# Kernel optimization log

Hardware: AMD Instinct MI355X
Metric: run time of the kernel (lower is better)

Reference implementation:

```python
import jax, jax.numpy as jnp
import numpy as np

B, N, F_IN, F_OUT = 8, 2048, 64, 64
ALPHA = 0.2
NEG = -9e15


def setup_inputs() -> dict:
    key = jax.random.key(0)
    k1, k2, k3, k4 = jax.random.split(key, 4)
    h = jax.random.normal(k1, (B, N, F_IN), dtype=jnp.float32)
    adj = jax.random.randint(k2, (N, N), 0, 2).astype(jnp.float32)
    W = jax.random.normal(k3, (F_OUT, F_IN), dtype=jnp.float32) * 0.05
    a = jax.random.normal(k4, (2 * F_OUT,), dtype=jnp.float32) * 0.05
    return {"h": h, "adj": adj, "W": W, "a": a}


def reference(h, adj, W, a):
    # Wh = h @ W^T  : [B, N, F_OUT]
    Wh = jnp.einsum("bnf,of->bno", h, W)
    # a([Wh_i, Wh_j]) decomposes exactly into a1.Wh_i + a2.Wh_j
    e1 = Wh @ a[:F_OUT]          # [B, N] contribution of source node i
    e2 = Wh @ a[F_OUT:]          # [B, N] contribution of target node j
    e = jax.nn.leaky_relu(e1[:, :, None] + e2[:, None, :], negative_slope=ALPHA)
    att = jnp.where(adj[None, :, :] > 0, e, NEG)
    att = jax.nn.softmax(att, axis=-1)   # [B, N, N]
    h_prime = jnp.einsum("bij,bjo->bio", att, Wh)
    return jax.nn.elu(h_prime)
```

## Files before the change

### kernel.cpp

```cpp
#include <hip/hip_runtime.h>
#include <hip/hip_bf16.h>
#include <math.h>


#define NN 2048
#define BB 8
#define ALPHA 0.2f

typedef __attribute__((ext_vector_type(8))) short s8v;
typedef __attribute__((ext_vector_type(4))) float f4v;

static __device__ __forceinline__ unsigned pk_bf16(float lo, float hi) {
  __hip_bfloat162 t = __float22bfloat162_rn(float2{lo, hi});
  return *(unsigned*)&t;
}

__global__ __launch_bounds__(256) void k_adj(const float* __restrict__ adj,
                                             unsigned long long* __restrict__ adjq) {
  const int t = threadIdx.x, lane = t & 63, w = t >> 6;
  const int row = blockIdx.x * 2 + (w >> 1);
  const int half = w & 1;
  const float* ar = adj + (size_t)row * NN + half * 1024;
  unsigned long long* aq = adjq + row * 32 + half * 16;
  #pragma unroll
  for (int it = 0; it < 16; ++it) {
    unsigned long long m = __ballot(ar[it * 64 + lane] > 0.f);
    if (lane == 0) aq[it] = m;
  }
}

__global__ __launch_bounds__(256, 2) void k_wh(
    const float* __restrict__ h, const float* __restrict__ W,
    const float* __restrict__ a, unsigned short* __restrict__ whtg,
    float* __restrict__ e1, float* __restrict__ e2) {
  __shared__ __align__(16) float hs[32][68];
  __shared__ __align__(16) unsigned short Ws[64][40];
  const int t = threadIdx.x, lane = t & 63, w = t >> 6;
  const int rowBase = blockIdx.x * 32;
  const int b = rowBase >> 11, n0 = rowBase & (NN - 1);

  float wr[64];
  #pragma unroll
  for (int k = 0; k < 16; ++k)
    *(f4v*)&wr[k * 4] = *(const f4v*)&W[lane * 64 + k * 4];

  #pragma unroll
  for (int qq = 0; qq < 2; ++qq) {
    const int idx = t + 256 * qq;
    const int r = idx >> 4, c = (idx & 15) * 4;
    *(f4v*)&hs[r][c] = *(const f4v*)&h[(size_t)(rowBase + r) * 64 + c];
  }
  const float a1v = a[lane], a2v = a[64 + lane];
  __syncthreads();

  const int r0 = w * 8;
  float acc[8];
  #pragma unroll
  for (int rr = 0; rr < 8; ++rr) acc[rr] = 0.f;
  #pragma unroll
  for (int f4i = 0; f4i < 16; ++f4i) {
    f4v hv[8];
    #pragma unroll
    for (int rr = 0; rr < 8; ++rr)
      hv[rr] = *(const f4v*)&hs[r0 + rr][f4i * 4];
    #pragma unroll
    for (int x = 0; x < 4; ++x) {
      const float wv = wr[f4i * 4 + x];
      #pragma unroll
      for (int rr = 0; rr < 8; ++rr) acc[rr] = fmaf(hv[rr][x], wv, acc[rr]);
    }
  }
  #pragma unroll
  for (int p = 0; p < 4; ++p)
    *(unsigned*)&Ws[lane][r0 + p * 2] = pk_bf16(acc[p * 2], acc[p * 2 + 1]);

  float s1[8], s2[8];
  #pragma unroll
  for (int rr = 0; rr < 8; ++rr) { s1[rr] = acc[rr] * a1v; s2[rr] = acc[rr] * a2v; }
  #pragma unroll
  for (int m = 1; m < 64; m <<= 1)
    #pragma unroll
    for (int rr = 0; rr < 8; ++rr) {
      s1[rr] += __shfl_xor(s1[rr], m);
      s2[rr] += __shfl_xor(s2[rr], m);
    }
  if (lane == 0)
    #pragma unroll
    for (int rr = 0; rr < 8; ++rr) {
      e1[rowBase + r0 + rr] = s1[rr];
      e2[rowBase + r0 + rr] = s2[rr];
    }
  __syncthreads();

  const int o = t >> 2, seg = t & 3;
  const s8v v = *(const s8v*)&Ws[o][seg * 8];
  *(s8v*)(whtg + ((size_t)(b * 64 + o) << 11) + n0 + seg * 8) = v;
}

__global__ __launch_bounds__(256, 2) void k_attn(
    const unsigned long long* __restrict__ adjq,
    const unsigned short* __restrict__ whtg,
    const float* __restrict__ e1g, const float* __restrict__ e2g,
    float* __restrict__ out) {
  __shared__ __align__(16) float e2row[NN];
  __shared__ __align__(16) float pc[4][16][68];
  __shared__ float ls[4][16];

  const int t = threadIdx.x, lane = t & 63, w = t >> 6;
  const int q = lane >> 4, l15 = lane & 15;
  const int b = blockIdx.y;
  const int i0 = blockIdx.x * 16;
  const size_t bN = (size_t)b * NN;

  #pragma unroll
  for (int kk = 0; kk < 2; ++kk) {
    const int idx = (t + 256 * kk) * 4;
    *(f4v*)&e2row[idx] = *(const f4v*)&e2g[bN + idx];
  }

  const float e1v = e1g[bN + i0 + l15];
  const unsigned long long* arow = adjq + (size_t)(i0 + l15) * 32 + w * 8;
  const unsigned short* wb = whtg + ((size_t)b << 17);
  const int jbase = w * 512;

  f4v acc[4];
  #pragma unroll
  for (int s = 0; s < 4; ++s) acc[s] = f4v{0.f, 0.f, 0.f, 0.f};
  float psum = 0.f;

  s8v bf[8];
  #pragma unroll
  for (int s = 0; s < 4; ++s)
    #pragma unroll
    for (int ks = 0; ks < 2; ++ks)
      bf[s * 2 + ks] =
          *(const s8v*)(wb + (((size_t)(s * 16 + l15)) << 11) + jbase + ks * 32 + q * 8);
  unsigned long long am = arow[0];

  __syncthreads();

  #pragma unroll
  for (int k = 0; k < 8; ++k) {
    const int j0 = jbase + k * 64;
    s8v cur[8];
    #pragma unroll
    for (int x = 0; x < 8; ++x) cur[x] = bf[x];
    const unsigned long long amc = am;
    if (k < 7) {
      const int jn = j0 + 64;
      #pragma unroll
      for (int s = 0; s < 4; ++s)
        #pragma unroll
        for (int ks = 0; ks < 2; ++ks)
          bf[s * 2 + ks] =
              *(const s8v*)(wb + (((size_t)(s * 16 + l15)) << 11) + jn + ks * 32 + q * 8);
      am = arow[k + 1];
    }

    s8v af[2];
    #pragma unroll
    for (int ks = 0; ks < 2; ++ks) {
      const unsigned bits = (unsigned)(amc >> (ks * 32 + q * 8)) & 0xffu;
      const f4v ea = *(const f4v*)&e2row[j0 + ks * 32 + q * 8];
      const f4v eb = *(const f4v*)&e2row[j0 + ks * 32 + q * 8 + 4];
      float p[8];
      #pragma unroll
      for (int jj = 0; jj < 8; ++jj) {
        const float s = e1v + (jj < 4 ? ea[jj & 3] : eb[jj & 3]);
        const float lr = fmaxf(s, ALPHA * s);
        const float pv = ((bits >> jj) & 1u) ? __expf(lr) : 0.f;
        p[jj] = pv;
        psum += pv;
      }
      union { s8v v; unsigned u[4]; } cv;
      cv.u[0] = pk_bf16(p[0], p[1]);
      cv.u[1] = pk_bf16(p[2], p[3]);
      cv.u[2] = pk_bf16(p[4], p[5]);
      cv.u[3] = pk_bf16(p[6], p[7]);
      af[ks] = cv.v;
    }

    #pragma unroll
    for (int s = 0; s < 4; ++s) {
      acc[s] = __builtin_amdgcn_mfma_f32_16x16x32_bf16(af[0], cur[s * 2 + 0], acc[s], 0, 0, 0);
      acc[s] = __builtin_amdgcn_mfma_f32_16x16x32_bf16(af[1], cur[s * 2 + 1], acc[s], 0, 0, 0);
    }
  }

  psum += __shfl_xor(psum, 16);
  psum += __shfl_xor(psum, 32);
  if (lane < 16) ls[w][lane] = psum;
  #pragma unroll
  for (int s = 0; s < 4; ++s)
    #pragma unroll
    for (int r = 0; r < 4; ++r)
      pc[w][q * 4 + r][s * 16 + l15] = acc[s][r];
  __syncthreads();

  const int row = t >> 4, c0 = (t & 15) * 4;
  f4v sum = *(const f4v*)&pc[0][row][c0];
  #pragma unroll
  for (int j = 1; j < 4; ++j) sum += *(const f4v*)&pc[j][row][c0];
  const float rsum = ls[0][row] + ls[1][row] + ls[2][row] + ls[3][row];
  f4v o;
  #pragma unroll
  for (int x = 0; x < 4; ++x) {
    float v = sum[x] / rsum;
    o[x] = v > 0.f ? v : expm1f(v);
  }
  *(f4v*)&out[(bN + i0 + row) * 64 + c0] = o;
}

extern "C" void kernel_launch(void* const* d_in, const int* in_sizes, int n_in,
                              void* d_out, int out_size, void* d_ws, size_t ws_size,
                              hipStream_t stream) {
  (void)in_sizes; (void)n_in; (void)out_size; (void)ws_size;
  const float* h   = (const float*)d_in[0];
  const float* adj = (const float*)d_in[1];
  const float* W   = (const float*)d_in[2];
  const float* a   = (const float*)d_in[3];
  float* outp = (float*)d_out;

  unsigned short* whtg = (unsigned short*)d_ws;
  float* e1 = (float*)((char*)d_ws + (size_t)BB * 64 * NN * 2);
  float* e2 = e1 + (size_t)BB * NN;
  unsigned long long* adjq = (unsigned long long*)(e2 + (size_t)BB * NN);

  k_adj<<<NN / 2, 256, 0, stream>>>(adj, adjq);
  k_wh<<<(BB * NN) / 32, 256, 0, stream>>>(h, W, a, whtg, e1, e2);
  k_attn<<<dim3(NN / 16, BB), 256, 0, stream>>>(adjq, whtg, e1, e2, outp);
}
```

Before: 118.3 us.

## Store Wh in MFMA-fragment-swizzled layout so attention loads are contiguous

The Wh projection kernel now writes its bf16 output straight into a layout that matches the MFMA B-fragment order of the attention kernel. This removes the LDS transpose and the extra barrier in k_wh. In k_attn each wave can then load its fragments as fully contiguous 16-byte-per-lane chunks instead of strided rows. The cost is a more intricate index mapping shared by producer and consumer, which must stay in sync.

```diff
diff --git a/kernel.cpp b/kernel.cpp
--- a/kernel.cpp
+++ b/kernel.cpp
@@ -31,13 +31,13 @@
 
 __global__ __launch_bounds__(256, 2) void k_wh(
     const float* __restrict__ h, const float* __restrict__ W,
-    const float* __restrict__ a, unsigned short* __restrict__ whtg,
+    const float* __restrict__ a, unsigned short* __restrict__ whswz,
     float* __restrict__ e1, float* __restrict__ e2) {
   __shared__ __align__(16) float hs[32][68];
-  __shared__ __align__(16) unsigned short Ws[64][40];
   const int t = threadIdx.x, lane = t & 63, w = t >> 6;
   const int rowBase = blockIdx.x * 32;
   const int b = rowBase >> 11, n0 = rowBase & (NN - 1);
+  const int jt = n0 >> 6, ks = (n0 >> 5) & 1;
 
   float wr[64];
   #pragma unroll
@@ -70,9 +70,18 @@
       for (int rr = 0; rr < 8; ++rr) acc[rr] = fmaf(hv[rr][x], wv, acc[rr]);
     }
   }
-  #pragma unroll
-  for (int p = 0; p < 4; ++p)
-    *(unsigned*)&Ws[lane][r0 + p * 2] = pk_bf16(acc[p * 2], acc[p * 2 + 1]);
+
+  {
+    union { s8v v; unsigned u[4]; } cv;
+    cv.u[0] = pk_bf16(acc[0], acc[1]);
+    cv.u[1] = pk_bf16(acc[2], acc[3]);
+    cv.u[2] = pk_bf16(acc[4], acc[5]);
+    cv.u[3] = pk_bf16(acc[6], acc[7]);
+    unsigned short* dst = whswz + ((size_t)b << 17) + (jt << 12) +
+                          ((((lane >> 4) << 1) + ks) << 9) +
+                          ((w * 16 + (lane & 15)) << 3);
+    *(s8v*)dst = cv.v;
+  }
 
   float s1[8], s2[8];
   #pragma unroll
@@ -90,16 +99,11 @@
       e1[rowBase + r0 + rr] = s1[rr];
       e2[rowBase + r0 + rr] = s2[rr];
     }
-  __syncthreads();
-
-  const int o = t >> 2, seg = t & 3;
-  const s8v v = *(const s8v*)&Ws[o][seg * 8];
-  *(s8v*)(whtg + ((size_t)(b * 64 + o) << 11) + n0 + seg * 8) = v;
 }
 
 __global__ __launch_bounds__(256, 2) void k_attn(
     const unsigned long long* __restrict__ adjq,
-    const unsigned short* __restrict__ whtg,
+    const unsigned short* __restrict__ whswz,
     const float* __restrict__ e1g, const float* __restrict__ e2g,
     float* __restrict__ out) {
   __shared__ __align__(16) float e2row[NN];
@@ -120,7 +124,7 @@
 
   const float e1v = e1g[bN + i0 + l15];
   const unsigned long long* arow = adjq + (size_t)(i0 + l15) * 32 + w * 8;
-  const unsigned short* wb = whtg + ((size_t)b << 17);
+  const unsigned short* tbase = whswz + ((size_t)b << 17) + ((size_t)(w * 8) << 12);
   const int jbase = w * 512;
 
   f4v acc[4];
@@ -130,11 +134,8 @@
 
   s8v bf[8];
   #pragma unroll
-  for (int s = 0; s < 4; ++s)
-    #pragma unroll
-    for (int ks = 0; ks < 2; ++ks)
-      bf[s * 2 + ks] =
-          *(const s8v*)(wb + (((size_t)(s * 16 + l15)) << 11) + jbase + ks * 32 + q * 8);
+  for (int f = 0; f < 8; ++f)
+    bf[f] = *(const s8v*)(tbase + (f << 9) + (lane << 3));
   unsigned long long am = arow[0];
 
   __syncthreads();
@@ -147,13 +148,10 @@
     for (int x = 0; x < 8; ++x) cur[x] = bf[x];
     const unsigned long long amc = am;
     if (k < 7) {
-      const int jn = j0 + 64;
+      const unsigned short* nb = tbase + ((k + 1) << 12);
       #pragma unroll
-      for (int s = 0; s < 4; ++s)
-        #pragma unroll
-        for (int ks = 0; ks < 2; ++ks)
-          bf[s * 2 + ks] =
-              *(const s8v*)(wb + (((size_t)(s * 16 + l15)) << 11) + jn + ks * 32 + q * 8);
+      for (int f = 0; f < 8; ++f)
+        bf[f] = *(const s8v*)(nb + (f << 9) + (lane << 3));
       am = arow[k + 1];
     }
 
@@ -221,12 +219,12 @@
   const float* a   = (const float*)d_in[3];
   float* outp = (float*)d_out;
 
-  unsigned short* whtg = (unsigned short*)d_ws;
+  unsigned short* whswz = (unsigned short*)d_ws;
   float* e1 = (float*)((char*)d_ws + (size_t)BB * 64 * NN * 2);
   float* e2 = e1 + (size_t)BB * NN;
   unsigned long long* adjq = (unsigned long long*)(e2 + (size_t)BB * NN);
 
   k_adj<<<NN / 2, 256, 0, stream>>>(adj, adjq);
-  k_wh<<<(BB * NN) / 32, 256, 0, stream>>>(h, W, a, whtg, e1, e2);
-  k_attn<<<dim3(NN / 16, BB), 256, 0, stream>>>(adjq, whtg, e1, e2, outp);
-}
+  k_wh<<<(BB * NN) / 32, 256, 0, stream>>>(h, W, a, whswz, e1, e2);
+  k_attn<<<dim3(NN / 16, BB), 256, 0, stream>>>(adjq, whswz, e1, e2, outp);
+}
```

After: 101.8 us. 1.16x faster.
